# Kernel optimization log

Measured on AMD Instinct MI355X. Metric: run time of the kernel, lower is better.

## Reference

```python
import jax, jax.numpy as jnp
import numpy as np

B, C, H, W = 16, 512, 32, 32
COND_C, L_COND = 768, 77
N_GROUPS, N_HEADS = 8, 8
HEAD = C // N_HEADS
EPS = 1e-5


def setup_inputs() -> dict:
    key = jax.random.key(0)
    ks = jax.random.split(key, 6)
    s = lambda fan_in: 1.0 / np.sqrt(fan_in)
    return {
        "x_0": jax.random.normal(ks[0], (B, C, H, W), jnp.float32),
        "cond": jax.random.normal(ks[1], (B, L_COND, COND_C), jnp.float32),
        "gn_gamma": jnp.ones((C,), jnp.float32),
        "gn_beta": jnp.zeros((C,), jnp.float32),
        "qkv_w": jax.random.normal(ks[2], (3 * C, C), jnp.float32) * s(C),
        "qkv_b": jnp.zeros((3 * C,), jnp.float32),
        "cond_kv_w": jax.random.normal(ks[3], (2 * C, COND_C), jnp.float32) * s(COND_C),
        "cond_kv_b": jnp.zeros((2 * C,), jnp.float32),
        "out_w": jax.random.normal(ks[4], (C, C), jnp.float32) * s(C),
        "out_b": jnp.zeros((C,), jnp.float32),
    }


def reference(x_0, cond, gn_gamma, gn_beta, qkv_w, qkv_b, cond_kv_w, cond_kv_b, out_w, out_b):
    b, c, h, w = x_0.shape
    L = h * w
    # --- GroupNorm over (C/G, H, W) per group, per-channel affine ---
    xg = x_0.reshape(b, N_GROUPS, c // N_GROUPS, h * w)
    mu = xg.mean(axis=(2, 3), keepdims=True)
    var = xg.var(axis=(2, 3), keepdims=True)
    xn = ((xg - mu) * jax.lax.rsqrt(var + EPS)).reshape(b, c, h, w)
    xn = xn * gn_gamma[None, :, None, None] + gn_beta[None, :, None, None]
    # --- to tokens [B, L, C] ---
    x = xn.transpose(0, 2, 3, 1).reshape(b, L, c)
    # --- QKV ---
    qkv = x @ qkv_w.T + qkv_b  # [B, L, 3C]
    q, k, v = jnp.split(qkv, 3, axis=-1)
    q = q.reshape(b, L, N_HEADS, HEAD)
    k = k.reshape(b, L, N_HEADS, HEAD)
    v = v.reshape(b, L, N_HEADS, HEAD)
    # --- conditional K/V ---
    kv_c = cond @ cond_kv_w.T + cond_kv_b  # [B, Lc, 2C]
    k_c, v_c = jnp.split(kv_c, 2, axis=-1)
    Lc = cond.shape[1]
    k_c = k_c.reshape(b, Lc, N_HEADS, HEAD)
    v_c = v_c.reshape(b, Lc, N_HEADS, HEAD)
    K = jnp.concatenate([k, k_c], axis=1)  # [B, L+Lc, H, D]
    V = jnp.concatenate([v, v_c], axis=1)
    # --- attention (full score matrix, as in the original) ---
    scale = HEAD ** -0.5
    scores = jnp.einsum("bqhd,bkhd->bhqk", q, K) * scale
    att = jax.nn.softmax(scores, axis=-1)
    out = jnp.einsum("bhqk,bkhd->bqhd", att, V).reshape(b, L, c)
    out = out @ out_w.T + out_b
    # --- back to image + residual ---
    out = out.reshape(b, h, w, c).transpose(0, 3, 1, 2)
    return out + x_0
```

## Files before the change

### kernel.cpp

```cpp
#include <hip/hip_runtime.h>

typedef short bf16x8 __attribute__((ext_vector_type(8)));
typedef float f32x4 __attribute__((ext_vector_type(4)));
typedef float f32x16 __attribute__((ext_vector_type(16)));
typedef unsigned int u32x4 __attribute__((ext_vector_type(4)));

#define KVP 1152

__device__ __forceinline__ unsigned short f2b(float f) {
    unsigned int u = __float_as_uint(f);
    u += 0x7FFFu + ((u >> 16) & 1u);
    return (unsigned short)(u >> 16);
}

__device__ __forceinline__ f32x4 mfma16(bf16x8 a, bf16x8 b, f32x4 c) {
    return __builtin_amdgcn_mfma_f32_16x16x32_bf16(a, b, c, 0, 0, 0);
}
__device__ __forceinline__ f32x16 mfma32(bf16x8 a, bf16x8 b, f32x16 c) {
    return __builtin_amdgcn_mfma_f32_32x32x16_bf16(a, b, c, 0, 0, 0);
}
__device__ __forceinline__ float exp2_raw(float x) {
    float r; asm("v_exp_f32 %0, %1" : "=v"(r) : "v"(x)); return r;
}
__device__ __forceinline__ unsigned cvt_pk(float lo, float hi) {
    unsigned r; asm("v_cvt_pk_bf16_f32 %0, %1, %2" : "=v"(r) : "v"(lo), "v"(hi)); return r;
}

typedef __attribute__((address_space(3))) unsigned int lds_u32_t;
typedef const __attribute__((address_space(1))) unsigned int glb_u32_t;
__device__ __forceinline__ void async_cp16(const void* g, void* l) {
    __builtin_amdgcn_global_load_lds((glb_u32_t*)(unsigned long long)g,
                                     (lds_u32_t*)(unsigned int)(unsigned long long)l,
                                     16, 0, 0);
}

__global__ __launch_bounds__(256) void gn_part_k(const float* __restrict__ x, float2* __restrict__ part) {
    int blk = blockIdx.x;
    const float4* p = (const float4*)(x + (size_t)blk * 16384);
    float s = 0.f, ss = 0.f;
    for (int i = threadIdx.x; i < 4096; i += 256) {
        float4 v = p[i];
        s  += v.x + v.y + v.z + v.w;
        ss += v.x * v.x + v.y * v.y + v.z * v.z + v.w * v.w;
    }
#pragma unroll
    for (int o = 32; o; o >>= 1) { s += __shfl_down(s, o); ss += __shfl_down(ss, o); }
    __shared__ float red[8];
    int w = threadIdx.x >> 6;
    if ((threadIdx.x & 63) == 0) { red[w] = s; red[4 + w] = ss; }
    __syncthreads();
    if (threadIdx.x == 0) {
        s  = red[0] + red[1] + red[2] + red[3];
        ss = red[4] + red[5] + red[6] + red[7];
        part[blk] = make_float2(s, ss);
    }
}

__global__ __launch_bounds__(256) void gn_apply_k(const float* __restrict__ x, const float2* __restrict__ part,
                                                  const float* __restrict__ gamma, const float* __restrict__ beta,
                                                  unsigned short* __restrict__ xt) {
    int st = blockIdx.x & 15;
    int ct = (blockIdx.x >> 4) & 7;
    int b  = blockIdx.x >> 7;
    int bg = b * 8 + ct;
    float2 p0 = part[4 * bg], p1 = part[4 * bg + 1], p2 = part[4 * bg + 2], p3 = part[4 * bg + 3];
    float s = (p0.x + p1.x) + (p2.x + p3.x);
    float ss = (p0.y + p1.y) + (p2.y + p3.y);
    float mean = s * (1.f / 65536.f);
    float var  = ss * (1.f / 65536.f) - mean * mean;
    float rsig = rsqrtf(var + 1e-5f);
    __shared__ unsigned short tile[64][65];
    int tid = threadIdx.x;
#pragma unroll
    for (int it = 0; it < 4; ++it) {
        int idx = it * 256 + tid;
        int ci = idx >> 4, j4 = idx & 15;
        int c = ct * 64 + ci;
        float4 v = *(const float4*)(x + ((size_t)b * 512 + c) * 1024 + st * 64 + j4 * 4);
        float gs = gamma[c] * rsig;
        float bo = beta[c] - mean * gs;
        tile[j4 * 4 + 0][ci] = f2b(v.x * gs + bo);
        tile[j4 * 4 + 1][ci] = f2b(v.y * gs + bo);
        tile[j4 * 4 + 2][ci] = f2b(v.z * gs + bo);
        tile[j4 * 4 + 3][ci] = f2b(v.w * gs + bo);
    }
    __syncthreads();
#pragma unroll
    for (int it = 0; it < 4; ++it) {
        int idx = it * 256 + tid;
        int si = idx >> 4, q = idx & 15;
        uint2 u;
        u.x = (unsigned)tile[si][q * 4 + 0] | ((unsigned)tile[si][q * 4 + 1] << 16);
        u.y = (unsigned)tile[si][q * 4 + 2] | ((unsigned)tile[si][q * 4 + 3] << 16);
        *(uint2*)(xt + ((size_t)b * 1024 + st * 64 + si) * 512 + ct * 64 + q * 4) = u;
    }
}

__global__ __launch_bounds__(256) void cvt_k(const float* __restrict__ in, unsigned short* __restrict__ out, int n4) {
    int i = blockIdx.x * 256 + threadIdx.x;
    if (i < n4) {
        float4 v = ((const float4*)in)[i];
        uint2 u;
        u.x = (unsigned)f2b(v.x) | ((unsigned)f2b(v.y) << 16);
        u.y = (unsigned)f2b(v.z) | ((unsigned)f2b(v.w) << 16);
        ((uint2*)out)[i] = u;
    }
}

template <int EPI>
__global__ __launch_bounds__(256) void gemm128_k(const unsigned short* __restrict__ A,
                                                 const unsigned short* __restrict__ Bw,
                                                 const float* __restrict__ bias,
                                                 int K,
                                                 unsigned short* __restrict__ Qo,
                                                 unsigned short* __restrict__ Ko,
                                                 unsigned short* __restrict__ Vo,
                                                 const float* __restrict__ x0,
                                                 float* __restrict__ outp) {
    __shared__ __align__(16) unsigned short As[3][4096];
    __shared__ __align__(16) unsigned short Bs[3][4096];
    const int m0 = blockIdx.x * 128, n0 = blockIdx.y * 128;
    const int tid = threadIdx.x, lane = tid & 63, w = tid >> 6;
    const int wr = w >> 1, wc = w & 1;
    const int lc = lane & 15, lg = lane >> 4;

    const int sRow = lane >> 2;
    const int sSlot = (lane & 3) ^ ((lane >> 3) & 3);
    const unsigned short* aSrc0 = A + (size_t)(m0 + 16 * w + sRow) * K + sSlot * 8;
    const unsigned short* aSrc1 = A + (size_t)(m0 + 64 + 16 * w + sRow) * K + sSlot * 8;
    const unsigned short* bSrc0 = Bw + (size_t)(n0 + 16 * w + sRow) * K + sSlot * 8;
    const unsigned short* bSrc1 = Bw + (size_t)(n0 + 64 + 16 * w + sRow) * K + sSlot * 8;

    const int rSlot8 = (lg ^ ((lc >> 1) & 3)) * 8;

    f32x4 acc[4][4];
#pragma unroll
    for (int m = 0; m < 4; ++m)
#pragma unroll
        for (int n = 0; n < 4; ++n) acc[m][n] = (f32x4){0.f, 0.f, 0.f, 0.f};

    const int nT = K >> 5;
    async_cp16(aSrc0, &As[0][w * 512]);
    async_cp16(aSrc1, &As[0][(4 + w) * 512]);
    async_cp16(bSrc0, &Bs[0][w * 512]);
    async_cp16(bSrc1, &Bs[0][(4 + w) * 512]);
    async_cp16(aSrc0 + 32, &As[1][w * 512]);
    async_cp16(aSrc1 + 32, &As[1][(4 + w) * 512]);
    async_cp16(bSrc0 + 32, &Bs[1][w * 512]);
    async_cp16(bSrc1 + 32, &Bs[1][(4 + w) * 512]);

    int c = 0;
#pragma unroll 1
    for (int t = 0; t < nT; ++t) {
        if (t + 2 < nT) {
            int c2 = c + 2; if (c2 >= 3) c2 -= 3;
            const int k2 = (t + 2) << 5;
            async_cp16(aSrc0 + k2, &As[c2][w * 512]);
            async_cp16(aSrc1 + k2, &As[c2][(4 + w) * 512]);
            async_cp16(bSrc0 + k2, &Bs[c2][w * 512]);
            async_cp16(bSrc1 + k2, &Bs[c2][(4 + w) * 512]);
            asm volatile("s_waitcnt vmcnt(8)" ::: "memory");
        } else if (t + 1 < nT) {
            asm volatile("s_waitcnt vmcnt(4)" ::: "memory");
        } else {
            asm volatile("s_waitcnt vmcnt(0)" ::: "memory");
        }
        __builtin_amdgcn_s_barrier();

        bf16x8 af[4], bfr[4];
#pragma unroll
        for (int m = 0; m < 4; ++m)
            af[m] = *(const bf16x8*)&As[c][(wr * 64 + m * 16 + lc) * 32 + rSlot8];
#pragma unroll
        for (int n = 0; n < 4; ++n)
            bfr[n] = *(const bf16x8*)&Bs[c][(wc * 64 + n * 16 + lc) * 32 + rSlot8];
        asm volatile("s_waitcnt lgkmcnt(0)" ::: "memory");
        __builtin_amdgcn_sched_barrier(0);
        __builtin_amdgcn_s_barrier();

#pragma unroll
        for (int m = 0; m < 4; ++m)
#pragma unroll
            for (int n = 0; n < 4; ++n) {
                if (EPI == 0) acc[m][n] = mfma16(bfr[n], af[m], acc[m][n]);
                else          acc[m][n] = mfma16(af[m], bfr[n], acc[m][n]);
            }

        ++c; if (c == 3) c = 0;
    }

    if (EPI == 0) {
        const bool isQ = (n0 < 512);
        const float sc = isQ ? (0.125f * 1.44269504089f) : 1.f;
#pragma unroll
        for (int n = 0; n < 4; ++n) {
            const int c0 = n0 + wc * 64 + n * 16 + lg * 4;
            const float4 b4 = *(const float4*)&bias[c0];
#pragma unroll
            for (int m = 0; m < 4; ++m) {
                const int tok = m0 + wr * 64 + m * 16 + lc;
                const int b = tok >> 10, l = tok & 1023;
                float v0 = (acc[m][n][0] + b4.x) * sc;
                float v1 = (acc[m][n][1] + b4.y) * sc;
                float v2 = (acc[m][n][2] + b4.z) * sc;
                float v3 = (acc[m][n][3] + b4.w) * sc;
                uint2 u = make_uint2(cvt_pk(v0, v1), cvt_pk(v2, v3));
                if (isQ) {
                    const int hh = c0 >> 6, d = c0 & 63;
                    *(uint2*)(Qo + ((size_t)(b * 8 + hh) * 1024 + l) * 64 + d) = u;
                } else {
                    const int hh = (c0 - 512) >> 6, d = c0 & 63;
                    *(uint2*)(Ko + ((size_t)(b * 8 + hh) * KVP + l) * 64 + d) = u;
                }
            }
        }
    } else if (EPI == 1) {
#pragma unroll
        for (int n = 0; n < 4; ++n) {
            const int j = n0 + wc * 64 + n * 16 + lc;
            const int hh = j >> 6, d = j & 63;
            const float bv = bias[j];
#pragma unroll
            for (int m = 0; m < 4; ++m) {
                const int t0 = m0 + wr * 64 + m * 16 + lg * 4;
                const int b = t0 >> 10, l0 = t0 & 1023;
                uint2 u = make_uint2(cvt_pk(acc[m][n][0] + bv, acc[m][n][1] + bv),
                                     cvt_pk(acc[m][n][2] + bv, acc[m][n][3] + bv));
                *(uint2*)(Vo + ((size_t)(b * 8 + hh) * 64 + d) * KVP + l0) = u;
            }
        }
    } else {
#pragma unroll
        for (int n = 0; n < 4; ++n) {
            const int col = n0 + wc * 64 + n * 16 + lc;
            const float bv = bias[col];
#pragma unroll
            for (int m = 0; m < 4; ++m) {
                const int t0 = m0 + wr * 64 + m * 16 + lg * 4;
                const size_t a = ((size_t)(t0 >> 10) * 512 + col) * 1024 + (t0 & 1023);
                float4 xv = *(const float4*)(x0 + a);
                float4 o;
                o.x = acc[m][n][0] + bv + xv.x;
                o.y = acc[m][n][1] + bv + xv.y;
                o.z = acc[m][n][2] + bv + xv.z;
                o.w = acc[m][n][3] + bv + xv.w;
                *(float4*)(outp + a) = o;
            }
        }
    }
}

__global__ __launch_bounds__(256) void gemm_nt_k(const unsigned short* __restrict__ A,
                                                 const unsigned short* __restrict__ Bw,
                                                 const float* __restrict__ bias,
                                                 int M, int N, int K,
                                                 unsigned short* __restrict__ Ko,
                                                 unsigned short* __restrict__ Vo) {
    __shared__ unsigned short As[64][40];
    __shared__ unsigned short Bs[64][40];
    const int m0 = blockIdx.x * 64, n0 = blockIdx.y * 64;
    const int tid = threadIdx.x, lane = tid & 63, w = tid >> 6;
    const int lc = lane & 15, lg = lane >> 4;
    const int lrow = tid >> 2, lseg = tid & 3;
    f32x4 acc[4];
#pragma unroll
    for (int i = 0; i < 4; ++i) acc[i] = (f32x4){0.f, 0.f, 0.f, 0.f};

    for (int k0 = 0; k0 < K; k0 += 32) {
        uint4 av = make_uint4(0u, 0u, 0u, 0u);
        if (m0 + lrow < M) av = *(const uint4*)(A + (size_t)(m0 + lrow) * K + k0 + lseg * 8);
        *(uint4*)&As[lrow][lseg * 8] = av;
        uint4 bv = *(const uint4*)(Bw + (size_t)(n0 + lrow) * K + k0 + lseg * 8);
        *(uint4*)&Bs[lrow][lseg * 8] = bv;
        __syncthreads();
        bf16x8 af = *(const bf16x8*)&As[w * 16 + lc][lg * 8];
#pragma unroll
        for (int ct = 0; ct < 4; ++ct) {
            bf16x8 bfr = *(const bf16x8*)&Bs[ct * 16 + lc][lg * 8];
            acc[ct] = mfma16(af, bfr, acc[ct]);
        }
        __syncthreads();
    }

    const int rbase = m0 + w * 16 + lg * 4;
#pragma unroll
    for (int ct = 0; ct < 4; ++ct) {
        int col = n0 + ct * 16 + lc;
        float bv = bias[col];
#pragma unroll
        for (int r = 0; r < 4; ++r) {
            int token = rbase + r;
            if (token >= M) continue;
            float val = acc[ct][r] + bv;
            int b = token / 77, l = token - b * 77;
            if (col < 512) {
                int hh = col >> 6, d = col & 63;
                Ko[((size_t)(b * 8 + hh) * KVP + 1024 + l) * 64 + d] = f2b(val);
            } else {
                int j = col - 512, hh = j >> 6, d = j & 63;
                Vo[((size_t)(b * 8 + hh) * 64 + d) * KVP + 1024 + l] = f2b(val);
            }
        }
    }
}

__global__ __launch_bounds__(512) void attn2_k(const unsigned short* __restrict__ Q,
                                               const unsigned short* __restrict__ Kb,
                                               const unsigned short* __restrict__ Vt,
                                               unsigned short* __restrict__ atok) {
    __shared__ __align__(16) unsigned short lds[18432];

    const int bh = blockIdx.x >> 2;
    const int qt = blockIdx.x & 3;
    const int w  = threadIdx.x >> 6;
    const int lane = threadIdx.x & 63;
    const int ql = lane & 31, hi = lane >> 5;
    const int q0 = qt * 256 + w * 32;

    bf16x8 qf[4];
    const unsigned short* Qp = Q + ((size_t)bh * 1024 + q0 + ql) * 64 + hi * 8;
#pragma unroll
    for (int ks = 0; ks < 4; ++ks) qf[ks] = *(const bf16x8*)(Qp + ks * 16);

    const unsigned short* Kg = Kb + (size_t)bh * KVP * 64;
    const unsigned short* Vg = Vt + (size_t)bh * 64 * KVP;

    const int srow = lane >> 3;
    const int sc   = (((lane & 7) ^ (lane >> 3)) << 3);

    f32x16 o0, o1;
#pragma unroll
    for (int i = 0; i < 16; ++i) { o0[i] = 0.f; o1[i] = 0.f; }
    float mreg = -1e30f, lsum = 0.f;

    {
        uint4 kr = *(const uint4*)(Kg + (size_t)(8 * w + srow) * 64 + sc);
        uint4 vr = *(const uint4*)(Vg + (size_t)(8 * w + srow) * KVP + sc);
        *(uint4*)&lds[w * 512 + lane * 8] = kr;
        *(uint4*)&lds[4096 + w * 512 + lane * 8] = vr;
    }
    __syncthreads();

    int cur = 0;
    for (int it = 0; it < 18; ++it) {
        const int kv0 = it * 64;
        const bool pre = (it < 17);
        uint4 kn, vn;
        if (pre) {
            kn = *(const uint4*)(Kg + (size_t)(kv0 + 64 + 8 * w + srow) * 64 + sc);
            vn = *(const uint4*)(Vg + (size_t)(8 * w + srow) * KVP + kv0 + 64 + sc);
        }
        const int kb = cur * 8192, vb = cur * 8192 + 4096;

        f32x16 s0, s1;
#pragma unroll
        for (int i = 0; i < 16; ++i) { s0[i] = 0.f; s1[i] = 0.f; }
#pragma unroll
        for (int ks = 0; ks < 4; ++ks) {
            const int sl = ((ks * 2 + hi) ^ (ql & 7)) << 3;
            bf16x8 kf0 = *(const bf16x8*)&lds[kb + ql * 64 + sl];
            bf16x8 kf1 = *(const bf16x8*)&lds[kb + (32 + ql) * 64 + sl];
            s0 = mfma32(kf0, qf[ks], s0);
            s1 = mfma32(kf1, qf[ks], s1);
        }
        if (kv0 == 1088) {
#pragma unroll
            for (int r = 0; r < 16; ++r) {
                int kva = 1088 + (r & 3) + 8 * (r >> 2) + 4 * hi;
                if (kva >= 1101) s0[r] = -1e30f;
                if (kva + 32 >= 1101) s1[r] = -1e30f;
            }
        }

        float t[16];
#pragma unroll
        for (int i = 0; i < 16; ++i) t[i] = fmaxf(s0[i], s1[i]);
#pragma unroll
        for (int st = 8; st; st >>= 1)
#pragma unroll
            for (int i = 0; i < st; ++i) t[i] = fmaxf(t[i], t[i + st]);
        float pmax = fmaxf(t[0], __shfl_xor(t[0], 32));

        if (__any(pmax > mreg + 8.f)) {
            float mn = fmaxf(mreg, pmax);
            float al = exp2_raw(mreg - mn);
            mreg = mn;
            lsum *= al;
#pragma unroll
            for (int i = 0; i < 16; ++i) { o0[i] *= al; o1[i] *= al; }
        }

        unsigned pk0[8], pk1[8];
        float sA = 0.f, sB = 0.f, sC = 0.f, sD = 0.f;
#pragma unroll
        for (int i = 0; i < 8; ++i) {
            float a0 = exp2_raw(s0[2 * i] - mreg), a1 = exp2_raw(s0[2 * i + 1] - mreg);
            float b0 = exp2_raw(s1[2 * i] - mreg), b1 = exp2_raw(s1[2 * i + 1] - mreg);
            pk0[i] = cvt_pk(a0, a1);
            pk1[i] = cvt_pk(b0, b1);
            sA += a0; sB += a1; sC += b0; sD += b1;
        }
        float ls = (sA + sB) + (sC + sD);
        ls += __shfl_xor(ls, 32);
        lsum += ls;

#pragma unroll
        for (int t2 = 0; t2 < 2; ++t2) {
            const unsigned* pk = t2 ? pk1 : pk0;
#pragma unroll
            for (int v = 0; v < 2; ++v) {
                unsigned a0 = pk[4 * v], a1 = pk[4 * v + 1], a2 = pk[4 * v + 2], a3 = pk[4 * v + 3];
                unsigned x = __shfl_xor(hi ? a0 : a2, 32);
                unsigned y = __shfl_xor(hi ? a1 : a3, 32);
                u32x4 fw;
                fw.x = hi ? x : a0; fw.y = hi ? y : a1; fw.z = hi ? a2 : x; fw.w = hi ? a3 : y;
                bf16x8 pf = __builtin_bit_cast(bf16x8, fw);
                const int ks2 = 2 * t2 + v;
                const int sl = ((ks2 * 2 + hi) ^ (ql & 7)) << 3;
                bf16x8 vf0 = *(const bf16x8*)&lds[vb + ql * 64 + sl];
                bf16x8 vf1 = *(const bf16x8*)&lds[vb + (32 + ql) * 64 + sl];
                o0 = mfma32(vf0, pf, o0);
                o1 = mfma32(vf1, pf, o1);
            }
        }

        if (pre) {
            *(uint4*)&lds[(cur ^ 1) * 8192 + w * 512 + lane * 8] = kn;
            *(uint4*)&lds[(cur ^ 1) * 8192 + 4096 + w * 512 + lane * 8] = vn;
        }
        __syncthreads();
        cur ^= 1;
    }

    float rinv = 1.f / lsum;
    unsigned short* sw = &lds[w * 2304];
#pragma unroll
    for (int dt = 0; dt < 2; ++dt) {
#pragma unroll
        for (int rp = 0; rp < 8; ++rp) {
            float e0 = (dt ? o1[2 * rp] : o0[2 * rp]) * rinv;
            float e1 = (dt ? o1[2 * rp + 1] : o0[2 * rp + 1]) * rinv;
            int d = dt * 32 + ((2 * rp) & 3) + 8 * ((2 * rp) >> 2) + 4 * hi;
            *(unsigned*)&sw[ql * 72 + d] = cvt_pk(e0, e1);
        }
    }
    __syncthreads();
    {
        int i = threadIdx.x >> 1, hf = threadIdx.x & 1;
        const unsigned short* src = &lds[(i >> 5) * 2304 + (i & 31) * 72 + hf * 32];
        u32x4 r0 = *(const u32x4*)(src);
        u32x4 r1 = *(const u32x4*)(src + 8);
        u32x4 r2 = *(const u32x4*)(src + 16);
        u32x4 r3 = *(const u32x4*)(src + 24);
        int b = bh >> 3, h = bh & 7;
        unsigned short* gd = atok + ((size_t)b * 1024 + qt * 256 + i) * 512 + h * 64 + hf * 32;
        *(u32x4*)(gd) = r0;
        *(u32x4*)(gd + 8) = r1;
        *(u32x4*)(gd + 16) = r2;
        *(u32x4*)(gd + 24) = r3;
    }
}

extern "C" void kernel_launch(void* const* d_in, const int* in_sizes, int n_in,
                              void* d_out, int out_size, void* d_ws, size_t ws_size,
                              hipStream_t stream) {
    const float* x0     = (const float*)d_in[0];
    const float* cond   = (const float*)d_in[1];
    const float* gamma  = (const float*)d_in[2];
    const float* beta   = (const float*)d_in[3];
    const float* qkv_w  = (const float*)d_in[4];
    const float* qkv_b  = (const float*)d_in[5];
    const float* ckv_w  = (const float*)d_in[6];
    const float* ckv_b  = (const float*)d_in[7];
    const float* out_w  = (const float*)d_in[8];
    const float* out_b  = (const float*)d_in[9];
    float* outp = (float*)d_out;

    char* p = (char*)d_ws;
    float2* part = (float2*)p;           p += 4096;
    unsigned short* xt    = (unsigned short*)p; p += (size_t)16384 * 512 * 2;
    unsigned short* wqkv  = (unsigned short*)p; p += (size_t)1536 * 512 * 2;
    unsigned short* wckv  = (unsigned short*)p; p += (size_t)1024 * 768 * 2;
    unsigned short* wout  = (unsigned short*)p; p += (size_t)512 * 512 * 2;
    unsigned short* condb = (unsigned short*)p; p += (size_t)1232 * 768 * 2;
    unsigned short* Qb    = (unsigned short*)p; p += (size_t)16 * 8 * 1024 * 64 * 2;
    unsigned short* Kb    = (unsigned short*)p; p += (size_t)16 * 8 * KVP * 64 * 2;
    unsigned short* Vtb   = (unsigned short*)p; p += (size_t)16 * 8 * KVP * 64 * 2;
    unsigned short* atok  = (unsigned short*)p; p += (size_t)16384 * 512 * 2;

    gn_part_k<<<512, 256, 0, stream>>>(x0, part);
    gn_apply_k<<<2048, 256, 0, stream>>>(x0, part, gamma, beta, xt);
    cvt_k<<<768, 256, 0, stream>>>(qkv_w, wqkv, 196608);
    cvt_k<<<768, 256, 0, stream>>>(ckv_w, wckv, 196608);
    cvt_k<<<256, 256, 0, stream>>>(out_w, wout, 65536);
    cvt_k<<<924, 256, 0, stream>>>(cond, condb, 236544);

    gemm128_k<0><<<dim3(128, 8), 256, 0, stream>>>(xt, wqkv, qkv_b, 512,
                                                   Qb, Kb, nullptr, nullptr, nullptr);
    gemm128_k<1><<<dim3(128, 4), 256, 0, stream>>>(xt, wqkv + (size_t)1024 * 512, qkv_b + 1024, 512,
                                                   nullptr, nullptr, Vtb, nullptr, nullptr);
    gemm_nt_k<<<dim3(20, 16), 256, 0, stream>>>(condb, wckv, ckv_b, 1232, 1024, 768, Kb, Vtb);
    attn2_k<<<512, 512, 0, stream>>>(Qb, Kb, Vtb, atok);
    gemm128_k<2><<<dim3(128, 4), 256, 0, stream>>>(atok, wout, out_b, 512,
                                                   nullptr, nullptr, nullptr, x0, outp);
}
```

Before: 179.7 us.

## Split attention into smaller 4-wave blocks, fuse weight conversions, add MFMA priority

The attention kernel now runs 1024 blocks of 4 waves (128 queries each) instead of 512 blocks of 8 waves, with each thread staging two K and two V rows. Blocks are remapped so neighbouring block IDs cover different batch-heads. Four separate fp32-to-bf16 conversion launches are merged into one kernel. s_setprio is raised around the MFMA sections to favour matrix issue. Smaller blocks may improve occupancy and tail balance, but each K/V tile is now loaded by twice as many blocks, doubling K/V traffic per query.

Result: slower. 184.7 us (+2.8%).

```diff
diff --git a/kernel.cpp b/kernel.cpp
--- a/kernel.cpp
+++ b/kernel.cpp
@@ -96,15 +96,20 @@
     }
 }
 
-__global__ __launch_bounds__(256) void cvt_k(const float* __restrict__ in, unsigned short* __restrict__ out, int n4) {
+__global__ __launch_bounds__(256) void cvtall_k(const float* __restrict__ a, unsigned short* __restrict__ oa,
+                                                const float* __restrict__ b, unsigned short* __restrict__ ob,
+                                                const float* __restrict__ c, unsigned short* __restrict__ oc,
+                                                const float* __restrict__ d, unsigned short* __restrict__ od) {
     int i = blockIdx.x * 256 + threadIdx.x;
-    if (i < n4) {
-        float4 v = ((const float4*)in)[i];
-        uint2 u;
-        u.x = (unsigned)f2b(v.x) | ((unsigned)f2b(v.y) << 16);
-        u.y = (unsigned)f2b(v.z) | ((unsigned)f2b(v.w) << 16);
-        ((uint2*)out)[i] = u;
-    }
+    const float* src; unsigned short* dst; int j;
+    if (i < 196608)      { src = a; dst = oa; j = i; }
+    else if (i < 393216) { src = b; dst = ob; j = i - 196608; }
+    else if (i < 458752) { src = c; dst = oc; j = i - 393216; }
+    else if (i < 695296) { src = d; dst = od; j = i - 458752; }
+    else return;
+    float4 v = ((const float4*)src)[j];
+    uint2 u = make_uint2(cvt_pk(v.x, v.y), cvt_pk(v.z, v.w));
+    ((uint2*)dst)[j] = u;
 }
 
 template <int EPI>
@@ -304,18 +309,19 @@
     }
 }
 
-__global__ __launch_bounds__(512) void attn2_k(const unsigned short* __restrict__ Q,
+__global__ __launch_bounds__(256) void attn3_k(const unsigned short* __restrict__ Q,
                                                const unsigned short* __restrict__ Kb,
                                                const unsigned short* __restrict__ Vt,
                                                unsigned short* __restrict__ atok) {
-    __shared__ __align__(16) unsigned short lds[18432];
-
-    const int bh = blockIdx.x >> 2;
-    const int qt = blockIdx.x & 3;
+    __shared__ __align__(16) unsigned short lds[16384];
+
+    const int bid = blockIdx.x;
+    const int bh = (bid & 7) * 16 + (bid >> 6);
+    const int qt = (bid >> 3) & 7;
     const int w  = threadIdx.x >> 6;
     const int lane = threadIdx.x & 63;
     const int ql = lane & 31, hi = lane >> 5;
-    const int q0 = qt * 256 + w * 32;
+    const int q0 = qt * 128 + w * 32;
 
     bf16x8 qf[4];
     const unsigned short* Qp = Q + ((size_t)bh * 1024 + q0 + ql) * 64 + hi * 8;
@@ -325,8 +331,9 @@
     const unsigned short* Kg = Kb + (size_t)bh * KVP * 64;
     const unsigned short* Vg = Vt + (size_t)bh * 64 * KVP;
 
-    const int srow = lane >> 3;
-    const int sc   = (((lane & 7) ^ (lane >> 3)) << 3);
+    const int sr  = threadIdx.x >> 3;
+    const int scN = threadIdx.x & 7;
+    const int off = ((scN ^ (sr & 7)) << 3);
 
     f32x16 o0, o1;
 #pragma unroll
@@ -334,10 +341,14 @@
     float mreg = -1e30f, lsum = 0.f;
 
     {
-        uint4 kr = *(const uint4*)(Kg + (size_t)(8 * w + srow) * 64 + sc);
-        uint4 vr = *(const uint4*)(Vg + (size_t)(8 * w + srow) * KVP + sc);
-        *(uint4*)&lds[w * 512 + lane * 8] = kr;
-        *(uint4*)&lds[4096 + w * 512 + lane * 8] = vr;
+        uint4 k1 = *(const uint4*)(Kg + (size_t)sr * 64 + off);
+        uint4 k2 = *(const uint4*)(Kg + (size_t)(32 + sr) * 64 + off);
+        uint4 v1 = *(const uint4*)(Vg + (size_t)sr * KVP + off);
+        uint4 v2 = *(const uint4*)(Vg + (size_t)(32 + sr) * KVP + off);
+        *(uint4*)&lds[sr * 64 + scN * 8] = k1;
+        *(uint4*)&lds[(32 + sr) * 64 + scN * 8] = k2;
+        *(uint4*)&lds[4096 + sr * 64 + scN * 8] = v1;
+        *(uint4*)&lds[4096 + (32 + sr) * 64 + scN * 8] = v2;
     }
     __syncthreads();
 
@@ -345,16 +356,19 @@
     for (int it = 0; it < 18; ++it) {
         const int kv0 = it * 64;
         const bool pre = (it < 17);
-        uint4 kn, vn;
+        uint4 kn1, kn2, vn1, vn2;
         if (pre) {
-            kn = *(const uint4*)(Kg + (size_t)(kv0 + 64 + 8 * w + srow) * 64 + sc);
-            vn = *(const uint4*)(Vg + (size_t)(8 * w + srow) * KVP + kv0 + 64 + sc);
+            kn1 = *(const uint4*)(Kg + (size_t)(kv0 + 64 + sr) * 64 + off);
+            kn2 = *(const uint4*)(Kg + (size_t)(kv0 + 96 + sr) * 64 + off);
+            vn1 = *(const uint4*)(Vg + (size_t)sr * KVP + kv0 + 64 + off);
+            vn2 = *(const uint4*)(Vg + (size_t)(32 + sr) * KVP + kv0 + 64 + off);
         }
         const int kb = cur * 8192, vb = cur * 8192 + 4096;
 
         f32x16 s0, s1;
 #pragma unroll
         for (int i = 0; i < 16; ++i) { s0[i] = 0.f; s1[i] = 0.f; }
+        __builtin_amdgcn_s_setprio(1);
 #pragma unroll
         for (int ks = 0; ks < 4; ++ks) {
             const int sl = ((ks * 2 + hi) ^ (ql & 7)) << 3;
@@ -363,6 +377,7 @@
             s0 = mfma32(kf0, qf[ks], s0);
             s1 = mfma32(kf1, qf[ks], s1);
         }
+        __builtin_amdgcn_s_setprio(0);
         if (kv0 == 1088) {
 #pragma unroll
             for (int r = 0; r < 16; ++r) {
@@ -419,14 +434,19 @@
                 const int sl = ((ks2 * 2 + hi) ^ (ql & 7)) << 3;
                 bf16x8 vf0 = *(const bf16x8*)&lds[vb + ql * 64 + sl];
                 bf16x8 vf1 = *(const bf16x8*)&lds[vb + (32 + ql) * 64 + sl];
+                __builtin_amdgcn_s_setprio(1);
                 o0 = mfma32(vf0, pf, o0);
                 o1 = mfma32(vf1, pf, o1);
+                __builtin_amdgcn_s_setprio(0);
             }
         }
 
         if (pre) {
-            *(uint4*)&lds[(cur ^ 1) * 8192 + w * 512 + lane * 8] = kn;
-            *(uint4*)&lds[(cur ^ 1) * 8192 + 4096 + w * 512 + lane * 8] = vn;
+            const int nb = (cur ^ 1) * 8192;
+            *(uint4*)&lds[nb + sr * 64 + scN * 8] = kn1;
+            *(uint4*)&lds[nb + (32 + sr) * 64 + scN * 8] = kn2;
+            *(uint4*)&lds[nb + 4096 + sr * 64 + scN * 8] = vn1;
+            *(uint4*)&lds[nb + 4096 + (32 + sr) * 64 + scN * 8] = vn2;
         }
         __syncthreads();
         cur ^= 1;
@@ -453,7 +473,7 @@
         u32x4 r2 = *(const u32x4*)(src + 16);
         u32x4 r3 = *(const u32x4*)(src + 24);
         int b = bh >> 3, h = bh & 7;
-        unsigned short* gd = atok + ((size_t)b * 1024 + qt * 256 + i) * 512 + h * 64 + hf * 32;
+        unsigned short* gd = atok + ((size_t)b * 1024 + qt * 128 + i) * 512 + h * 64 + hf * 32;
         *(u32x4*)(gd) = r0;
         *(u32x4*)(gd + 8) = r1;
         *(u32x4*)(gd + 16) = r2;
@@ -490,17 +510,14 @@
 
     gn_part_k<<<512, 256, 0, stream>>>(x0, part);
     gn_apply_k<<<2048, 256, 0, stream>>>(x0, part, gamma, beta, xt);
-    cvt_k<<<768, 256, 0, stream>>>(qkv_w, wqkv, 196608);
-    cvt_k<<<768, 256, 0, stream>>>(ckv_w, wckv, 196608);
-    cvt_k<<<256, 256, 0, stream>>>(out_w, wout, 65536);
-    cvt_k<<<924, 256, 0, stream>>>(cond, condb, 236544);
+    cvtall_k<<<2716, 256, 0, stream>>>(qkv_w, wqkv, ckv_w, wckv, out_w, wout, cond, condb);
 
     gemm128_k<0><<<dim3(128, 8), 256, 0, stream>>>(xt, wqkv, qkv_b, 512,
                                                    Qb, Kb, nullptr, nullptr, nullptr);
     gemm128_k<1><<<dim3(128, 4), 256, 0, stream>>>(xt, wqkv + (size_t)1024 * 512, qkv_b + 1024, 512,
                                                    nullptr, nullptr, Vtb, nullptr, nullptr);
     gemm_nt_k<<<dim3(20, 16), 256, 0, stream>>>(condb, wckv, ckv_b, 1232, 1024, 768, Kb, Vtb);
-    attn2_k<<<512, 512, 0, stream>>>(Qb, Kb, Vtb, atok);
+    attn3_k<<<1024, 256, 0, stream>>>(Qb, Kb, Vtb, atok);
     gemm128_k<2><<<dim3(128, 4), 256, 0, stream>>>(atok, wout, out_b, 512,
                                                    nullptr, nullptr, nullptr, x0, outp);
 }
```
